# Performance work log

Hardware: AMD Instinct MI355X
Metric: run time of the kernel (lower is better)

The kernel has to match this reference:

```python
import jax, jax.numpy as jnp
import numpy as np

SOS_TOKEN = 1


def gru_cell(x, h, Wih, Whh, bih, bhh):
    # torch.nn.GRU gate math; x:[B,H], h:[B,H]; Wih/Whh:[3H,H]
    gi = x @ Wih.T + bih
    gh = h @ Whh.T + bhh
    ir, iz, inn = jnp.split(gi, 3, axis=-1)
    hr, hz, hn = jnp.split(gh, 3, axis=-1)
    r = jax.nn.sigmoid(ir + hr)
    z = jax.nn.sigmoid(iz + hz)
    n = jnp.tanh(inn + r * hn)
    return (1.0 - z) * n + z * h


def setup_inputs() -> dict:
    key = jax.random.key(0)
    ks = jax.random.split(key, 20)
    B, S, T, V, H = 32, 512, 128, 32000, 512
    sc = 0.08
    p = lambda i, shape: (jax.random.normal(ks[i], shape, jnp.float32) * sc)
    return {
        "input_seq": jax.random.randint(ks[0], (B, S), 0, V),
        "target_seq": jax.random.randint(ks[1], (B, T), 0, V),
        "emb": p(2, (V, H)),
        "ef_Wih": p(3, (3 * H, H)), "ef_Whh": p(4, (3 * H, H)),
        "ef_bih": p(5, (3 * H,)), "ef_bhh": p(6, (3 * H,)),
        "eb_Wih": p(7, (3 * H, H)), "eb_Whh": p(8, (3 * H, H)),
        "eb_bih": p(9, (3 * H,)), "eb_bhh": p(10, (3 * H,)),
        "d_Wih": p(11, (3 * H, H)), "d_Whh": p(12, (3 * H, H)),
        "d_bih": p(13, (3 * H,)), "d_bhh": p(14, (3 * H,)),
        "att_W": p(15, (H, 2 * H)), "att_b": p(16, (H,)),
        "out_W": p(17, (V, H)), "out_b": p(18, (V,)),
    }


def reference(input_seq, target_seq, emb,
              ef_Wih, ef_Whh, ef_bih, ef_bhh,
              eb_Wih, eb_Whh, eb_bih, eb_bhh,
              d_Wih, d_Whh, d_bih, d_bhh,
              att_W, att_b, out_W, out_b):
    B, S = input_seq.shape
    T = target_seq.shape[1]
    H = emb.shape[1]
    dtype = emb.dtype

    # ---- encoder: bidirectional GRU over source ----
    xs = jnp.swapaxes(emb[input_seq], 0, 1)  # [S,B,H]
    h0 = jnp.zeros((B, H), dtype)

    def make_step(Wih, Whh, bih, bhh):
        def f(h, xt):
            hn = gru_cell(xt, h, Wih, Whh, bih, bhh)
            return hn, hn
        return f

    hf_last, out_f = jax.lax.scan(make_step(ef_Wih, ef_Whh, ef_bih, ef_bhh), h0, xs)
    hb_last, out_bwd = jax.lax.scan(make_step(eb_Wih, eb_Whh, eb_bih, eb_bhh), h0, xs[::-1])
    out_bwd = out_bwd[::-1]
    # encoder_output[:, :H] + encoder_output[:, H:]  == sum of directions
    enc_out = jnp.swapaxes(out_f + out_bwd, 0, 1)  # [B,S,H]
    # decoder_hidden = encoder_hidden[-1,0] + encoder_hidden[-1,1]
    h_dec0 = hf_last + hb_last  # [B,H]

    # ---- greedy decode for T steps with argmax feedback ----
    tgt = target_seq.T  # [T,B]
    tok0 = jnp.full((B,), SOS_TOKEN, target_seq.dtype)
    batch_idx = jnp.arange(B)

    def dec_step(carry, tgt_t):
        h, tok, loss = carry
        xt = emb[tok]                                   # [B,H]
        hn = gru_cell(xt, h, d_Wih, d_Whh, d_bih, d_bhh)
        scores = jnp.einsum('bh,bsh->bs', hn, enc_out)  # dot attention
        w = jax.nn.softmax(scores, axis=-1)
        ctx = jnp.einsum('bs,bsh->bh', w, enc_out)
        att_out = jnp.tanh(jnp.concatenate([ctx, hn], axis=-1) @ att_W.T + att_b)
        logits = att_out @ out_W.T + out_b              # [B,V]
        logp = jax.nn.log_softmax(logits, axis=-1)
        loss = loss - logp[batch_idx, tgt_t]            # -log softmax(output)[target]
        nxt = jnp.argmax(logits, axis=-1).astype(tok.dtype)
        return (hn, nxt, loss), None

    init = (h_dec0, tok0, jnp.zeros((B,), dtype))
    (_, _, loss), _ = jax.lax.scan(dec_step, init, tgt)
    # mean over examples of (per-example loss / decoding_cnt)
    return jnp.mean(loss / T)
```

## Files before the change

kernel.cpp:

```cpp
#include <hip/hip_runtime.h>
#include <math.h>

#define B 32
#define S 512
#define T 128
#define V 32000
#define H 512
#define NB 256
#define NT 256
#define LCHUNK 250
#define LROWS 128
#define LDSPITCH 264

__device__ __forceinline__ float dot4(float acc, float4 a, float4 b){
    return fmaf(a.x,b.x, fmaf(a.y,b.y, fmaf(a.z,b.z, fmaf(a.w,b.w, acc))));
}
__device__ __forceinline__ float sigmoidf_(float x){ return 1.0f/(1.0f+expf(-x)); }

template<int GRPSZ>
__device__ __forceinline__ void gbar_arrive(unsigned* bb, unsigned grp, unsigned n){
    __syncthreads();
    if (threadIdx.x == 0){
        const unsigned r = __hip_atomic_fetch_add(bb + grp*32, 1u,
                              __ATOMIC_RELEASE, __HIP_MEMORY_SCOPE_AGENT);
        if (r == n*(unsigned)GRPSZ - 1u){
            const unsigned q = __hip_atomic_fetch_add(bb + 256, 1u,
                                  __ATOMIC_RELEASE, __HIP_MEMORY_SCOPE_AGENT);
            if (q == n*8u - 1u)
                __hip_atomic_store(bb + 288, n,
                                   __ATOMIC_RELEASE, __HIP_MEMORY_SCOPE_AGENT);
        }
    }
}
__device__ __forceinline__ void gbar_wait(unsigned* bb, unsigned n){
    if (threadIdx.x == 0){
        long guard = 0;
        while (__hip_atomic_load(bb + 288, __ATOMIC_RELAXED, __HIP_MEMORY_SCOPE_AGENT) < n){
            __builtin_amdgcn_s_sleep(2);
            if (++guard > 200000000L) break;
        }
        (void)__hip_atomic_load(bb + 288, __ATOMIC_ACQUIRE, __HIP_MEMORY_SCOPE_AGENT);
    }
    __syncthreads();
}

__global__ __launch_bounds__(NT, 1) void enc_persistent(
    const int* __restrict__ input_seq, const float* __restrict__ emb,
    const float* __restrict__ fWih, const float* __restrict__ fWhh,
    const float* __restrict__ fbih, const float* __restrict__ fbhh,
    const float* __restrict__ bWih, const float* __restrict__ bWhh,
    const float* __restrict__ bbih, const float* __restrict__ bbhh,
    float* enc_out, float* out_b, unsigned* bars)
{
    __shared__ float wlds[24*512];
    __shared__ float shp[128*6];
    const int bk = blockIdx.x, tid = threadIdx.x;
    const int dir = bk & 1, jg = bk >> 1;
    const int b = tid & 31, jj = (tid>>5)&3, kh = tid>>7;
    const int j = jg*4 + jj;
    const unsigned grp = ((unsigned)jg) & 7u;

    const float *Wih = dir? bWih : fWih;
    const float *Whh = dir? bWhh : fWhh;
    const float *bih = dir? bbih : fbih;
    const float *bhh = dir? bbhh : fbhh;
    float* outp = dir? out_b : enc_out;
    unsigned* bar = bars + dir*1024;

    for (int r=0;r<24;r++){
        const int jr = jg*4 + (r/6);
        const int g  = r % 6;
        const float* src = (g<3) ? (Wih + ((size_t)g*H + jr)*H)
                                 : (Whh + ((size_t)(g-3)*H + jr)*H);
        for (int k=tid;k<H;k+=NT) wlds[r*512+k] = src[k];
    }
    __syncthreads();

    const float4* wx0 = (const float4*)(wlds + (jj*6+0)*512 + kh*256);
    const float4* wx1 = (const float4*)(wlds + (jj*6+1)*512 + kh*256);
    const float4* wx2 = (const float4*)(wlds + (jj*6+2)*512 + kh*256);
    const float4* wh0 = (const float4*)(wlds + (jj*6+3)*512 + kh*256);
    const float4* wh1 = (const float4*)(wlds + (jj*6+4)*512 + kh*256);
    const float4* wh2 = (const float4*)(wlds + (jj*6+5)*512 + kh*256);
    const float bi_r = bih[j], bi_z = bih[H+j], bi_n = bih[2*H+j];
    const float bh_r = bhh[j], bh_z = bhh[H+j], bh_n = bhh[2*H+j];

    for (int t=0; t<S; t++){
        const int pos  = dir ? (S-1-t) : t;
        const int hpos = dir ? (S-t)   : (t-1);
        const int tokb = input_seq[b*S + pos];
        const float4* x4 = (const float4*)(emb + (size_t)tokb*H + kh*256);

        float ir=0.f, iz=0.f, in_=0.f;
        #pragma unroll 4
        for (int k=0;k<64;k++){
            const float4 xv = x4[k];
            ir  = dot4(ir , xv, wx0[k]);
            iz  = dot4(iz , xv, wx1[k]);
            in_ = dot4(in_, xv, wx2[k]);
        }

        if (t > 0) gbar_wait(bar, (unsigned)t);

        float hr=0.f, hz=0.f, hn=0.f;
        if (t > 0){
            const float4* h4 = (const float4*)(outp + ((size_t)b*S + hpos)*H + kh*256);
            #pragma unroll 4
            for (int k=0;k<64;k++){
                const float4 hv = h4[k];
                hr = dot4(hr, hv, wh0[k]);
                hz = dot4(hz, hv, wh1[k]);
                hn = dot4(hn, hv, wh2[k]);
            }
        }
        if (kh){
            float* p = shp + (jj*32 + b)*6;
            p[0]=ir; p[1]=iz; p[2]=in_; p[3]=hr; p[4]=hz; p[5]=hn;
        }
        __syncthreads();
        if (!kh){
            const float* p = shp + (jj*32 + b)*6;
            ir+=p[0]; iz+=p[1]; in_+=p[2]; hr+=p[3]; hz+=p[4]; hn+=p[5];
            float hprev = (t>0) ? outp[((size_t)b*S + hpos)*H + j] : 0.0f;
            const float r = sigmoidf_(ir + bi_r + hr + bh_r);
            const float z = sigmoidf_(iz + bi_z + hz + bh_z);
            const float n = tanhf(in_ + bi_n + r*(hn + bh_n));
            outp[((size_t)b*S + pos)*H + j] = (1.0f - z)*n + z*hprev;
        }
        gbar_arrive<16>(bar, grp, (unsigned)(t+1));
    }
}

__global__ __launch_bounds__(NT, 1) void dec_persistent(
    const int* __restrict__ target_seq, const float* __restrict__ emb,
    const float* __restrict__ dWih, const float* __restrict__ dWhh,
    const float* __restrict__ dbih, const float* __restrict__ dbhh,
    const float* __restrict__ attW, const float* __restrict__ attb,
    const float* __restrict__ outW, const float* __restrict__ outBias,
    float* enc_out, const float* out_b,
    float* hdec, float* scores, float* ctxb, float* att_out,
    float* pm, float* ps, int* pidx, float* lossb,
    float* out, unsigned* bar)
{
    __shared__ __align__(16) float smem[32*LDSPITCH];
    __shared__ float wg[12*512];
    __shared__ float wp[2*1024];
    __shared__ int sh_tok[B];
    const int bk = blockIdx.x, tid = threadIdx.x;
    const unsigned grp = (unsigned)bk & 7u;
    unsigned bn = 1;
#define GSYNC() do { gbar_arrive<32>(bar, grp, bn); gbar_wait(bar, bn); ++bn; } while(0)

    for (int r=0;r<12;r++){
        const int jr = bk*2 + (r/6);
        const int g  = r % 6;
        const float* src = (g<3) ? (dWih + ((size_t)g*H + jr)*H)
                                 : (dWhh + ((size_t)(g-3)*H + jr)*H);
        for (int k=tid;k<H;k+=NT) wg[r*512+k] = src[k];
    }
    for (int r=0;r<2;r++){
        const float* src = attW + (size_t)(bk*2+r)*(2*H);
        for (int k=tid;k<2*H;k+=NT) wp[r*1024+k] = src[k];
    }

    {
        const int gid = bk*NT + tid;
        if (gid < B*H){
            const int bb = gid >> 9, jq = gid & 511;
            hdec[gid] = enc_out[((size_t)bb*S + (S-1))*H + jq] + out_b[((size_t)bb*S)*H + jq];
        }
        if (bk==0 && tid<B) lossb[tid] = 0.0f;
    }
    GSYNC();

    {
        float4* e4 = (float4*)enc_out; const float4* o4 = (const float4*)out_b;
        for (size_t i = (size_t)bk*NT + tid; i < (size_t)B*S*H/4; i += (size_t)NB*NT){
            float4 x = e4[i]; const float4 y = o4[i];
            x.x+=y.x; x.y+=y.y; x.z+=y.z; x.w+=y.w; e4[i]=x;
        }
    }
    GSYNC();

    const int gb = tid & 31, gj = (tid>>5)&1, gkq = tid>>6;
    const int jrow = bk*2 + gj;
    const float4* gwir = (const float4*)(wg + (gj*6+0)*512 + gkq*128);
    const float4* gwiz = (const float4*)(wg + (gj*6+1)*512 + gkq*128);
    const float4* gwin = (const float4*)(wg + (gj*6+2)*512 + gkq*128);
    const float4* gwhr = (const float4*)(wg + (gj*6+3)*512 + gkq*128);
    const float4* gwhz = (const float4*)(wg + (gj*6+4)*512 + gkq*128);
    const float4* gwhn = (const float4*)(wg + (gj*6+5)*512 + gkq*128);
    const float gbi_r = dbih[jrow], gbi_z = dbih[H+jrow], gbi_n = dbih[2*H+jrow];
    const float gbh_r = dbhh[jrow], gbh_z = dbhh[H+jrow], gbh_n = dbhh[2*H+jrow];
    const float4* pw = (const float4*)(wp + gj*1024 + gkq*256);

    for (int t=0; t<T; t++){
        float* hin  = hdec + (size_t)(t&1)*B*H;
        float* hout = hdec + (size_t)((t+1)&1)*B*H;

        if (t == 0){
            if (tid < B) sh_tok[tid] = 1;
        } else {
            const int mb = tid>>3, p = tid&7;
            float bv = -INFINITY; int ai = 0x7FFFFFFF;
            for (int c=p; c<LCHUNK; c+=8){
                const float v = pm[mb*LCHUNK + c];
                if (v > bv){ bv = v; ai = pidx[mb*LCHUNK + c]; }
            }
            #pragma unroll
            for (int m=1; m<8; m<<=1){
                const float ov = __shfl_xor(bv, m); const int oi = __shfl_xor(ai, m);
                if (ov > bv || (ov == bv && oi < ai)){ bv = ov; ai = oi; }
            }
            if (p==0) sh_tok[mb] = ai;
            if (bk == 0){
                float mm = -INFINITY;
                for (int c=p; c<LCHUNK; c+=8) mm = fmaxf(mm, pm[mb*LCHUNK+c]);
                #pragma unroll
                for (int m=1;m<8;m<<=1) mm = fmaxf(mm, __shfl_xor(mm, m));
                float se = 0.0f;
                for (int c=p; c<LCHUNK; c+=8) se += ps[mb*LCHUNK+c]*expf(pm[mb*LCHUNK+c]-mm);
                #pragma unroll
                for (int m=1;m<8;m<<=1) se += __shfl_xor(se, m);
                const int tg = target_seq[mb*T + (t-1)];
                const float4* ar = (const float4*)(att_out + (size_t)mb*H) + p*16;
                const float4* wr = (const float4*)(outW + (size_t)tg*H) + p*16;
                float d = 0.0f;
                #pragma unroll
                for (int k=0;k<16;k++) d = dot4(d, ar[k], wr[k]);
                #pragma unroll
                for (int m=1;m<8;m<<=1) d += __shfl_xor(d, m);
                if (p==0) lossb[mb] += (mm + logf(se)) - (d + outBias[tg]);
            }
        }
        __syncthreads();
        {
            const int tokb = sh_tok[gb];
            const float4* x4 = (const float4*)(emb + (size_t)tokb*H + gkq*128);
            const float4* h4 = (const float4*)(hin + (size_t)gb*H + gkq*128);
            float ir=0.f, iz=0.f, in_=0.f, hr=0.f, hz=0.f, hn=0.f;
            #pragma unroll 4
            for (int k=0;k<32;k++){
                const float4 xv = x4[k], hv = h4[k];
                ir  = dot4(ir , xv, gwir[k]);
                iz  = dot4(iz , xv, gwiz[k]);
                in_ = dot4(in_, xv, gwin[k]);
                hr  = dot4(hr , hv, gwhr[k]);
                hz  = dot4(hz , hv, gwhz[k]);
                hn  = dot4(hn , hv, gwhn[k]);
            }
            if (gkq){
                float* pp = smem + ((gkq-1)*64 + gj*32 + gb)*6;
                pp[0]=ir; pp[1]=iz; pp[2]=in_; pp[3]=hr; pp[4]=hz; pp[5]=hn;
            }
            __syncthreads();
            if (!gkq){
                #pragma unroll
                for (int q=0;q<3;q++){
                    const float* pp = smem + (q*64 + gj*32 + gb)*6;
                    ir+=pp[0]; iz+=pp[1]; in_+=pp[2]; hr+=pp[3]; hz+=pp[4]; hn+=pp[5];
                }
                const float r = sigmoidf_(ir + gbi_r + hr + gbh_r);
                const float z = sigmoidf_(iz + gbi_z + hz + gbh_z);
                const float n = tanhf(in_ + gbi_n + r*(hn + gbh_n));
                const float hprev = hin[(size_t)gb*H + jrow];
                hout[(size_t)gb*H + jrow] = (1.0f - z)*n + z*hprev;
            }
        }
        GSYNC();

        {
            const int bS = bk & 31, sg = bk >> 5;
            const int sl = tid>>2, q = tid&3;
            const int s = sg*64 + sl;
            const float4* h4 = (const float4*)(hout + (size_t)bS*H + q*128);
            const float4* e4 = (const float4*)(enc_out + ((size_t)bS*S + s)*H + q*128);
            float a = 0.f;
            #pragma unroll 8
            for (int k=0;k<32;k++) a = dot4(a, h4[k], e4[k]);
            a += __shfl_xor(a, 1);
            a += __shfl_xor(a, 2);
            if (q == 0) scores[bS*S + s] = a;
        }
        GSYNC();

        {
            const int bC = bk & 31, cg = bk >> 5;
            float* sh_w = smem; float* red = smem + 512; float* part = smem + 768;
            const float s0 = scores[bC*S + tid], s1 = scores[bC*S + tid + 256];
            red[tid] = fmaxf(s0,s1); __syncthreads();
            for (int off=128; off>0; off>>=1){ if (tid<off) red[tid]=fmaxf(red[tid],red[tid+off]); __syncthreads(); }
            const float M = red[0]; __syncthreads();
            const float e0 = expf(s0-M), e1 = expf(s1-M);
            red[tid] = e0+e1; __syncthreads();
            for (int off=128; off>0; off>>=1){ if (tid<off) red[tid]+=red[tid+off]; __syncthreads(); }
            const float inv = 1.0f/red[0];
            __syncthreads();
            sh_w[tid] = e0*inv; sh_w[tid+256] = e1*inv;
            __syncthreads();
            const int col = cg*64 + (tid & 63);
            const int sg2 = tid >> 6;
            const float* Ec = enc_out + (size_t)bC*S*H + col;
            float acc = 0.f;
            #pragma unroll 8
            for (int s2=sg2; s2<S; s2+=4) acc = fmaf(sh_w[s2], Ec[(size_t)s2*H], acc);
            part[tid] = acc; __syncthreads();
            if (tid < 64) ctxb[bC*512 + col] = part[tid]+part[tid+64]+part[tid+128]+part[tid+192];
        }
        GSYNC();

        {
            const float* act = (gkq < 2) ? (ctxb + (size_t)gb*512 + gkq*256)
                                         : (hout + (size_t)gb*H + (gkq-2)*256);
            const float4* a4 = (const float4*)act;
            float acc = 0.f;
            #pragma unroll 8
            for (int k=0;k<64;k++) acc = dot4(acc, a4[k], pw[k]);
            if (gkq){
                smem[(gkq-1)*64 + gj*32 + gb] = acc;
            }
            __syncthreads();
            if (!gkq){
                acc += smem[0*64 + gj*32 + gb] + smem[1*64 + gj*32 + gb] + smem[2*64 + gj*32 + gb];
                att_out[(size_t)gb*H + jrow] = tanhf(acc + attb[jrow]);
            }
        }
        GSYNC();

        if (bk < LCHUNK){
            const int rg = tid & 31, bg = tid >> 5;
            const int r0 = bk*LROWS + rg;
            const float4* w0 = (const float4*)(outW + (size_t)(r0     )*H);
            const float4* w1 = (const float4*)(outW + (size_t)(r0 + 32)*H);
            const float4* w2 = (const float4*)(outW + (size_t)(r0 + 64)*H);
            const float4* w3 = (const float4*)(outW + (size_t)(r0 + 96)*H);
            float4* sh4 = (float4*)smem;
            float acc[4][4];
            #pragma unroll
            for (int i=0;i<4;i++){ acc[i][0]=0.f; acc[i][1]=0.f; acc[i][2]=0.f; acc[i][3]=0.f; }

            for (int ph=0; ph<2; ph++){
                #pragma unroll
                for (int ii=0; ii<8; ii++){
                    const int f4 = tid + 256*ii;
                    const int bb = f4 >> 6, k4 = f4 & 63;
                    sh4[bb*(LDSPITCH/4) + k4] = ((const float4*)att_out)[(size_t)bb*(H/4) + ph*64 + k4];
                }
                __syncthreads();
                #pragma unroll 4
                for (int k=0;k<64;k++){
                    const float4 a0 = sh4[(bg*4+0)*(LDSPITCH/4) + k];
                    const float4 a1 = sh4[(bg*4+1)*(LDSPITCH/4) + k];
                    const float4 a2 = sh4[(bg*4+2)*(LDSPITCH/4) + k];
                    const float4 a3 = sh4[(bg*4+3)*(LDSPITCH/4) + k];
                    const int kk = ph*64 + k;
                    {   const float4 wv = w0[kk];
                        acc[0][0]=dot4(acc[0][0],wv,a0); acc[0][1]=dot4(acc[0][1],wv,a1);
                        acc[0][2]=dot4(acc[0][2],wv,a2); acc[0][3]=dot4(acc[0][3],wv,a3); }
                    {   const float4 wv = w1[kk];
                        acc[1][0]=dot4(acc[1][0],wv,a0); acc[1][1]=dot4(acc[1][1],wv,a1);
                        acc[1][2]=dot4(acc[1][2],wv,a2); acc[1][3]=dot4(acc[1][3],wv,a3); }
                    {   const float4 wv = w2[kk];
                        acc[2][0]=dot4(acc[2][0],wv,a0); acc[2][1]=dot4(acc[2][1],wv,a1);
                        acc[2][2]=dot4(acc[2][2],wv,a2); acc[2][3]=dot4(acc[2][3],wv,a3); }
                    {   const float4 wv = w3[kk];
                        acc[3][0]=dot4(acc[3][0],wv,a0); acc[3][1]=dot4(acc[3][1],wv,a1);
                        acc[3][2]=dot4(acc[3][2],wv,a2); acc[3][3]=dot4(acc[3][3],wv,a3); }
                }
                __syncthreads();
            }

            const float bias0 = outBias[r0], bias1 = outBias[r0+32], bias2 = outBias[r0+64], bias3 = outBias[r0+96];
            #pragma unroll
            for (int jb=0;jb<4;jb++){
                float l0 = acc[0][jb]+bias0, l1 = acc[1][jb]+bias1, l2 = acc[2][jb]+bias2, l3 = acc[3][jb]+bias3;
                float M = fmaxf(fmaxf(l0,l1), fmaxf(l2,l3));
                #pragma unroll
                for (int m=1;m<32;m<<=1) M = fmaxf(M, __shfl_xor(M, m));
                float sum = expf(l0-M)+expf(l1-M)+expf(l2-M)+expf(l3-M);
                #pragma unroll
                for (int m=1;m<32;m<<=1) sum += __shfl_xor(sum, m);
                float bv = l0; int bi = r0;
                if (l1 > bv){ bv=l1; bi=r0+32; }
                if (l2 > bv){ bv=l2; bi=r0+64; }
                if (l3 > bv){ bv=l3; bi=r0+96; }
                #pragma unroll
                for (int m=1;m<32;m<<=1){
                    const float ov = __shfl_xor(bv, m); const int oi = __shfl_xor(bi, m);
                    if (ov > bv || (ov == bv && oi < bi)){ bv=ov; bi=oi; }
                }
                if (rg == 0){
                    const int bb = bg*4 + jb;
                    pm[bb*LCHUNK + bk] = M;
                    ps[bb*LCHUNK + bk] = sum;
                    pidx[bb*LCHUNK + bk] = bi;
                }
            }
        }
        GSYNC();
    }

    if (bk == 0){
        const int mb = tid>>3, p = tid&7;
        float mm = -INFINITY;
        for (int c=p; c<LCHUNK; c+=8) mm = fmaxf(mm, pm[mb*LCHUNK+c]);
        #pragma unroll
        for (int m=1;m<8;m<<=1) mm = fmaxf(mm, __shfl_xor(mm, m));
        float se = 0.0f;
        for (int c=p; c<LCHUNK; c+=8) se += ps[mb*LCHUNK+c]*expf(pm[mb*LCHUNK+c]-mm);
        #pragma unroll
        for (int m=1;m<8;m<<=1) se += __shfl_xor(se, m);
        const int tg = target_seq[mb*T + (T-1)];
        const float4* ar = (const float4*)(att_out + (size_t)mb*H) + p*16;
        const float4* wr = (const float4*)(outW + (size_t)tg*H) + p*16;
        float d = 0.0f;
        #pragma unroll
        for (int k=0;k<16;k++) d = dot4(d, ar[k], wr[k]);
        #pragma unroll
        for (int m=1;m<8;m<<=1) d += __shfl_xor(d, m);
        if (p==0) lossb[mb] += (mm + logf(se)) - (d + outBias[tg]);
        __syncthreads();
        if (tid < B){
            float v = lossb[tid];
            for (int off=16; off>0; off>>=1) v += __shfl_down(v, off);
            if (tid == 0) out[0] = v / (float)(B*T);
        }
    }
#undef GSYNC
}

extern "C" void kernel_launch(void* const* d_in, const int* in_sizes, int n_in,
                              void* d_out, int out_size, void* d_ws, size_t ws_size,
                              hipStream_t stream)
{
    const int*   input_seq  = (const int*)  d_in[0];
    const int*   target_seq = (const int*)  d_in[1];
    const float* emb    = (const float*)d_in[2];
    const float* efWih  = (const float*)d_in[3];
    const float* efWhh  = (const float*)d_in[4];
    const float* efbih  = (const float*)d_in[5];
    const float* efbhh  = (const float*)d_in[6];
    const float* ebWih  = (const float*)d_in[7];
    const float* ebWhh  = (const float*)d_in[8];
    const float* ebbih  = (const float*)d_in[9];
    const float* ebbhh  = (const float*)d_in[10];
    const float* dWih   = (const float*)d_in[11];
    const float* dWhh   = (const float*)d_in[12];
    const float* dbih   = (const float*)d_in[13];
    const float* dbhh   = (const float*)d_in[14];
    const float* attW   = (const float*)d_in[15];
    const float* attb   = (const float*)d_in[16];
    const float* outW   = (const float*)d_in[17];
    const float* outBias= (const float*)d_in[18];

    float* ws      = (float*)d_ws;
    unsigned* bars = (unsigned*)ws;
    float* enc_out = ws + 4096;
    float* outb    = enc_out + (size_t)B*S*H;
    float* scores  = outb    + (size_t)B*S*H;
    float* ctxb    = scores  + (size_t)B*S;
    float* attout  = ctxb    + (size_t)B*512;
    float* pm      = attout  + (size_t)B*H;
    float* ps      = pm      + (size_t)B*LCHUNK;
    int*   pidx    = (int*)(ps + (size_t)B*LCHUNK);
    float* hdec    = (float*)(pidx + (size_t)B*LCHUNK);
    float* lossb   = hdec    + (size_t)2*B*H;

    hipMemsetAsync(bars, 0, 16384, stream);

    enc_persistent<<<NB, NT, 0, stream>>>(input_seq, emb,
        efWih, efWhh, efbih, efbhh, ebWih, ebWhh, ebbih, ebbhh,
        enc_out, outb, bars);

    dec_persistent<<<NB, NT, 0, stream>>>(target_seq, emb,
        dWih, dWhh, dbih, dbhh, attW, attb, outW, outBias,
        enc_out, outb, hdec, scores, ctxb, attout,
        pm, ps, pidx, lossb, (float*)d_out, bars + 2048);
}
```

Measured before the change: 32.41 ms.

## Double threads per block and split reduction dimensions across more threads

Raises the block size of the persistent encoder and decoder kernels from 256 to 512 threads. Each phase (GRU gate dot products, attention scores, softmax/context, attention projection, vocab logits) is re-partitioned so each thread covers half as much of the K or S dimension, with larger shared-memory partial reductions. The aim is to shorten the per-step critical path of these latency-bound recurrent loops by adding intra-block parallelism. The cost is more shared-memory reduction work and possible register or occupancy pressure, and some sections must now guard threads 256 and above.

```diff
diff --git a/kernel.cpp b/kernel.cpp
--- a/kernel.cpp
+++ b/kernel.cpp
@@ -7,7 +7,7 @@
 #define V 32000
 #define H 512
 #define NB 256
-#define NT 256
+#define NT 512
 #define LCHUNK 250
 #define LROWS 128
 #define LDSPITCH 264
@@ -53,7 +53,7 @@
     float* enc_out, float* out_b, unsigned* bars)
 {
     __shared__ float wlds[24*512];
-    __shared__ float shp[128*6];
+    __shared__ float shp[3*128*6];
     const int bk = blockIdx.x, tid = threadIdx.x;
     const int dir = bk & 1, jg = bk >> 1;
     const int b = tid & 31, jj = (tid>>5)&3, kh = tid>>7;
@@ -76,12 +76,12 @@
     }
     __syncthreads();
 
-    const float4* wx0 = (const float4*)(wlds + (jj*6+0)*512 + kh*256);
-    const float4* wx1 = (const float4*)(wlds + (jj*6+1)*512 + kh*256);
-    const float4* wx2 = (const float4*)(wlds + (jj*6+2)*512 + kh*256);
-    const float4* wh0 = (const float4*)(wlds + (jj*6+3)*512 + kh*256);
-    const float4* wh1 = (const float4*)(wlds + (jj*6+4)*512 + kh*256);
-    const float4* wh2 = (const float4*)(wlds + (jj*6+5)*512 + kh*256);
+    const float4* wx0 = (const float4*)(wlds + (jj*6+0)*512 + kh*128);
+    const float4* wx1 = (const float4*)(wlds + (jj*6+1)*512 + kh*128);
+    const float4* wx2 = (const float4*)(wlds + (jj*6+2)*512 + kh*128);
+    const float4* wh0 = (const float4*)(wlds + (jj*6+3)*512 + kh*128);
+    const float4* wh1 = (const float4*)(wlds + (jj*6+4)*512 + kh*128);
+    const float4* wh2 = (const float4*)(wlds + (jj*6+5)*512 + kh*128);
     const float bi_r = bih[j], bi_z = bih[H+j], bi_n = bih[2*H+j];
     const float bh_r = bhh[j], bh_z = bhh[H+j], bh_n = bhh[2*H+j];
 
@@ -89,11 +89,11 @@
         const int pos  = dir ? (S-1-t) : t;
         const int hpos = dir ? (S-t)   : (t-1);
         const int tokb = input_seq[b*S + pos];
-        const float4* x4 = (const float4*)(emb + (size_t)tokb*H + kh*256);
+        const float4* x4 = (const float4*)(emb + (size_t)tokb*H + kh*128);
 
         float ir=0.f, iz=0.f, in_=0.f;
-        #pragma unroll 4
-        for (int k=0;k<64;k++){
+        #pragma unroll 8
+        for (int k=0;k<32;k++){
             const float4 xv = x4[k];
             ir  = dot4(ir , xv, wx0[k]);
             iz  = dot4(iz , xv, wx1[k]);
@@ -104,9 +104,9 @@
 
         float hr=0.f, hz=0.f, hn=0.f;
         if (t > 0){
-            const float4* h4 = (const float4*)(outp + ((size_t)b*S + hpos)*H + kh*256);
-            #pragma unroll 4
-            for (int k=0;k<64;k++){
+            const float4* h4 = (const float4*)(outp + ((size_t)b*S + hpos)*H + kh*128);
+            #pragma unroll 8
+            for (int k=0;k<32;k++){
                 const float4 hv = h4[k];
                 hr = dot4(hr, hv, wh0[k]);
                 hz = dot4(hz, hv, wh1[k]);
@@ -114,13 +114,16 @@
             }
         }
         if (kh){
-            float* p = shp + (jj*32 + b)*6;
+            float* p = shp + ((kh-1)*128 + jj*32 + b)*6;
             p[0]=ir; p[1]=iz; p[2]=in_; p[3]=hr; p[4]=hz; p[5]=hn;
         }
         __syncthreads();
         if (!kh){
-            const float* p = shp + (jj*32 + b)*6;
-            ir+=p[0]; iz+=p[1]; in_+=p[2]; hr+=p[3]; hz+=p[4]; hn+=p[5];
+            #pragma unroll
+            for (int q=0;q<3;q++){
+                const float* p = shp + (q*128 + jj*32 + b)*6;
+                ir+=p[0]; iz+=p[1]; in_+=p[2]; hr+=p[3]; hz+=p[4]; hn+=p[5];
+            }
             float hprev = (t>0) ? outp[((size_t)b*S + hpos)*H + j] : 0.0f;
             const float r = sigmoidf_(ir + bi_r + hr + bh_r);
             const float z = sigmoidf_(iz + bi_z + hz + bh_z);
@@ -184,15 +187,15 @@
 
     const int gb = tid & 31, gj = (tid>>5)&1, gkq = tid>>6;
     const int jrow = bk*2 + gj;
-    const float4* gwir = (const float4*)(wg + (gj*6+0)*512 + gkq*128);
-    const float4* gwiz = (const float4*)(wg + (gj*6+1)*512 + gkq*128);
-    const float4* gwin = (const float4*)(wg + (gj*6+2)*512 + gkq*128);
-    const float4* gwhr = (const float4*)(wg + (gj*6+3)*512 + gkq*128);
-    const float4* gwhz = (const float4*)(wg + (gj*6+4)*512 + gkq*128);
-    const float4* gwhn = (const float4*)(wg + (gj*6+5)*512 + gkq*128);
+    const float4* gwir = (const float4*)(wg + (gj*6+0)*512 + gkq*64);
+    const float4* gwiz = (const float4*)(wg + (gj*6+1)*512 + gkq*64);
+    const float4* gwin = (const float4*)(wg + (gj*6+2)*512 + gkq*64);
+    const float4* gwhr = (const float4*)(wg + (gj*6+3)*512 + gkq*64);
+    const float4* gwhz = (const float4*)(wg + (gj*6+4)*512 + gkq*64);
+    const float4* gwhn = (const float4*)(wg + (gj*6+5)*512 + gkq*64);
     const float gbi_r = dbih[jrow], gbi_z = dbih[H+jrow], gbi_n = dbih[2*H+jrow];
     const float gbh_r = dbhh[jrow], gbh_z = dbhh[H+jrow], gbh_n = dbhh[2*H+jrow];
-    const float4* pw = (const float4*)(wp + gj*1024 + gkq*256);
+    const float4* pw = (const float4*)(wp + gj*1024 + gkq*128);
 
     for (int t=0; t<T; t++){
         float* hin  = hdec + (size_t)(t&1)*B*H;
@@ -200,7 +203,7 @@
 
         if (t == 0){
             if (tid < B) sh_tok[tid] = 1;
-        } else {
+        } else if (tid < 256) {
             const int mb = tid>>3, p = tid&7;
             float bv = -INFINITY; int ai = 0x7FFFFFFF;
             for (int c=p; c<LCHUNK; c+=8){
@@ -236,11 +239,11 @@
         __syncthreads();
         {
             const int tokb = sh_tok[gb];
-            const float4* x4 = (const float4*)(emb + (size_t)tokb*H + gkq*128);
-            const float4* h4 = (const float4*)(hin + (size_t)gb*H + gkq*128);
+            const float4* x4 = (const float4*)(emb + (size_t)tokb*H + gkq*64);
+            const float4* h4 = (const float4*)(hin + (size_t)gb*H + gkq*64);
             float ir=0.f, iz=0.f, in_=0.f, hr=0.f, hz=0.f, hn=0.f;
-            #pragma unroll 4
-            for (int k=0;k<32;k++){
+            #pragma unroll
+            for (int k=0;k<16;k++){
                 const float4 xv = x4[k], hv = h4[k];
                 ir  = dot4(ir , xv, gwir[k]);
                 iz  = dot4(iz , xv, gwiz[k]);
@@ -256,7 +259,7 @@
             __syncthreads();
             if (!gkq){
                 #pragma unroll
-                for (int q=0;q<3;q++){
+                for (int q=0;q<7;q++){
                     const float* pp = smem + (q*64 + gj*32 + gb)*6;
                     ir+=pp[0]; iz+=pp[1]; in_+=pp[2]; hr+=pp[3]; hz+=pp[4]; hn+=pp[5];
                 }
@@ -271,57 +274,64 @@
 
         {
             const int bS = bk & 31, sg = bk >> 5;
-            const int sl = tid>>2, q = tid&3;
+            const int sl = tid>>3, q = tid&7;
             const int s = sg*64 + sl;
-            const float4* h4 = (const float4*)(hout + (size_t)bS*H + q*128);
-            const float4* e4 = (const float4*)(enc_out + ((size_t)bS*S + s)*H + q*128);
+            const float4* h4 = (const float4*)(hout + (size_t)bS*H + q*64);
+            const float4* e4 = (const float4*)(enc_out + ((size_t)bS*S + s)*H + q*64);
             float a = 0.f;
-            #pragma unroll 8
-            for (int k=0;k<32;k++) a = dot4(a, h4[k], e4[k]);
+            #pragma unroll
+            for (int k=0;k<16;k++) a = dot4(a, h4[k], e4[k]);
             a += __shfl_xor(a, 1);
             a += __shfl_xor(a, 2);
+            a += __shfl_xor(a, 4);
             if (q == 0) scores[bS*S + s] = a;
         }
         GSYNC();
 
         {
             const int bC = bk & 31, cg = bk >> 5;
-            float* sh_w = smem; float* red = smem + 512; float* part = smem + 768;
-            const float s0 = scores[bC*S + tid], s1 = scores[bC*S + tid + 256];
-            red[tid] = fmaxf(s0,s1); __syncthreads();
-            for (int off=128; off>0; off>>=1){ if (tid<off) red[tid]=fmaxf(red[tid],red[tid+off]); __syncthreads(); }
+            float* sh_w = smem; float* red = smem + 512; float* part = smem + 1024;
+            const float s0 = scores[bC*S + tid];
+            red[tid] = s0; __syncthreads();
+            for (int off=256; off>0; off>>=1){ if (tid<off) red[tid]=fmaxf(red[tid],red[tid+off]); __syncthreads(); }
             const float M = red[0]; __syncthreads();
-            const float e0 = expf(s0-M), e1 = expf(s1-M);
-            red[tid] = e0+e1; __syncthreads();
-            for (int off=128; off>0; off>>=1){ if (tid<off) red[tid]+=red[tid+off]; __syncthreads(); }
+            const float e0 = expf(s0-M);
+            red[tid] = e0; __syncthreads();
+            for (int off=256; off>0; off>>=1){ if (tid<off) red[tid]+=red[tid+off]; __syncthreads(); }
             const float inv = 1.0f/red[0];
             __syncthreads();
-            sh_w[tid] = e0*inv; sh_w[tid+256] = e1*inv;
+            sh_w[tid] = e0*inv;
             __syncthreads();
             const int col = cg*64 + (tid & 63);
             const int sg2 = tid >> 6;
             const float* Ec = enc_out + (size_t)bC*S*H + col;
             float acc = 0.f;
             #pragma unroll 8
-            for (int s2=sg2; s2<S; s2+=4) acc = fmaf(sh_w[s2], Ec[(size_t)s2*H], acc);
+            for (int s2=sg2; s2<S; s2+=8) acc = fmaf(sh_w[s2], Ec[(size_t)s2*H], acc);
             part[tid] = acc; __syncthreads();
-            if (tid < 64) ctxb[bC*512 + col] = part[tid]+part[tid+64]+part[tid+128]+part[tid+192];
+            if (tid < 64){
+                float v = 0.f;
+                #pragma unroll
+                for (int i=0;i<8;i++) v += part[tid + 64*i];
+                ctxb[bC*512 + cg*64 + tid] = v;
+            }
         }
         GSYNC();
 
         {
-            const float* act = (gkq < 2) ? (ctxb + (size_t)gb*512 + gkq*256)
-                                         : (hout + (size_t)gb*H + (gkq-2)*256);
+            const float* act = (gkq < 4) ? (ctxb + (size_t)gb*512 + gkq*128)
+                                         : (hout + (size_t)gb*H + (gkq-4)*128);
             const float4* a4 = (const float4*)act;
             float acc = 0.f;
-            #pragma unroll 8
-            for (int k=0;k<64;k++) acc = dot4(acc, a4[k], pw[k]);
+            #pragma unroll
+            for (int k=0;k<32;k++) acc = dot4(acc, a4[k], pw[k]);
             if (gkq){
                 smem[(gkq-1)*64 + gj*32 + gb] = acc;
             }
             __syncthreads();
             if (!gkq){
-                acc += smem[0*64 + gj*32 + gb] + smem[1*64 + gj*32 + gb] + smem[2*64 + gj*32 + gb];
+                #pragma unroll
+                for (int q=0;q<7;q++) acc += smem[q*64 + gj*32 + gb];
                 att_out[(size_t)gb*H + jrow] = tanhf(acc + attb[jrow]);
             }
         }
@@ -335,44 +345,38 @@
             const float4* w2 = (const float4*)(outW + (size_t)(r0 + 64)*H);
             const float4* w3 = (const float4*)(outW + (size_t)(r0 + 96)*H);
             float4* sh4 = (float4*)smem;
-            float acc[4][4];
-            #pragma unroll
-            for (int i=0;i<4;i++){ acc[i][0]=0.f; acc[i][1]=0.f; acc[i][2]=0.f; acc[i][3]=0.f; }
+            float acc[4][2];
+            #pragma unroll
+            for (int i=0;i<4;i++){ acc[i][0]=0.f; acc[i][1]=0.f; }
 
             for (int ph=0; ph<2; ph++){
                 #pragma unroll
-                for (int ii=0; ii<8; ii++){
-                    const int f4 = tid + 256*ii;
+                for (int ii=0; ii<4; ii++){
+                    const int f4 = tid + 512*ii;
                     const int bb = f4 >> 6, k4 = f4 & 63;
                     sh4[bb*(LDSPITCH/4) + k4] = ((const float4*)att_out)[(size_t)bb*(H/4) + ph*64 + k4];
                 }
                 __syncthreads();
                 #pragma unroll 4
                 for (int k=0;k<64;k++){
-                    const float4 a0 = sh4[(bg*4+0)*(LDSPITCH/4) + k];
-                    const float4 a1 = sh4[(bg*4+1)*(LDSPITCH/4) + k];
-                    const float4 a2 = sh4[(bg*4+2)*(LDSPITCH/4) + k];
-                    const float4 a3 = sh4[(bg*4+3)*(LDSPITCH/4) + k];
+                    const float4 a0 = sh4[(bg*2+0)*(LDSPITCH/4) + k];
+                    const float4 a1 = sh4[(bg*2+1)*(LDSPITCH/4) + k];
                     const int kk = ph*64 + k;
                     {   const float4 wv = w0[kk];
-                        acc[0][0]=dot4(acc[0][0],wv,a0); acc[0][1]=dot4(acc[0][1],wv,a1);
-                        acc[0][2]=dot4(acc[0][2],wv,a2); acc[0][3]=dot4(acc[0][3],wv,a3); }
+                        acc[0][0]=dot4(acc[0][0],wv,a0); acc[0][1]=dot4(acc[0][1],wv,a1); }
                     {   const float4 wv = w1[kk];
-                        acc[1][0]=dot4(acc[1][0],wv,a0); acc[1][1]=dot4(acc[1][1],wv,a1);
-                        acc[1][2]=dot4(acc[1][2],wv,a2); acc[1][3]=dot4(acc[1][3],wv,a3); }
+                        acc[1][0]=dot4(acc[1][0],wv,a0); acc[1][1]=dot4(acc[1][1],wv,a1); }
                     {   const float4 wv = w2[kk];
-                        acc[2][0]=dot4(acc[2][0],wv,a0); acc[2][1]=dot4(acc[2][1],wv,a1);
-                        acc[2][2]=dot4(acc[2][2],wv,a2); acc[2][3]=dot4(acc[2][3],wv,a3); }
+                        acc[2][0]=dot4(acc[2][0],wv,a0); acc[2][1]=dot4(acc[2][1],wv,a1); }
                     {   const float4 wv = w3[kk];
-                        acc[3][0]=dot4(acc[3][0],wv,a0); acc[3][1]=dot4(acc[3][1],wv,a1);
-                        acc[3][2]=dot4(acc[3][2],wv,a2); acc[3][3]=dot4(acc[3][3],wv,a3); }
+                        acc[3][0]=dot4(acc[3][0],wv,a0); acc[3][1]=dot4(acc[3][1],wv,a1); }
                 }
                 __syncthreads();
             }
 
             const float bias0 = outBias[r0], bias1 = outBias[r0+32], bias2 = outBias[r0+64], bias3 = outBias[r0+96];
             #pragma unroll
-            for (int jb=0;jb<4;jb++){
+            for (int jb=0;jb<2;jb++){
                 float l0 = acc[0][jb]+bias0, l1 = acc[1][jb]+bias1, l2 = acc[2][jb]+bias2, l3 = acc[3][jb]+bias3;
                 float M = fmaxf(fmaxf(l0,l1), fmaxf(l2,l3));
                 #pragma unroll
@@ -390,7 +394,7 @@
                     if (ov > bv || (ov == bv && oi < bi)){ bv=ov; bi=oi; }
                 }
                 if (rg == 0){
-                    const int bb = bg*4 + jb;
+                    const int bb = bg*2 + jb;
                     pm[bb*LCHUNK + bk] = M;
                     ps[bb*LCHUNK + bk] = sum;
                     pidx[bb*LCHUNK + bk] = bi;
@@ -401,24 +405,26 @@
     }
 
     if (bk == 0){
-        const int mb = tid>>3, p = tid&7;
-        float mm = -INFINITY;
-        for (int c=p; c<LCHUNK; c+=8) mm = fmaxf(mm, pm[mb*LCHUNK+c]);
-        #pragma unroll
-        for (int m=1;m<8;m<<=1) mm = fmaxf(mm, __shfl_xor(mm, m));
-        float se = 0.0f;
-        for (int c=p; c<LCHUNK; c+=8) se += ps[mb*LCHUNK+c]*expf(pm[mb*LCHUNK+c]-mm);
-        #pragma unroll
-        for (int m=1;m<8;m<<=1) se += __shfl_xor(se, m);
-        const int tg = target_seq[mb*T + (T-1)];
-        const float4* ar = (const float4*)(att_out + (size_t)mb*H) + p*16;
-        const float4* wr = (const float4*)(outW + (size_t)tg*H) + p*16;
-        float d = 0.0f;
-        #pragma unroll
-        for (int k=0;k<16;k++) d = dot4(d, ar[k], wr[k]);
-        #pragma unroll
-        for (int m=1;m<8;m<<=1) d += __shfl_xor(d, m);
-        if (p==0) lossb[mb] += (mm + logf(se)) - (d + outBias[tg]);
+        if (tid < 256){
+            const int mb = tid>>3, p = tid&7;
+            float mm = -INFINITY;
+            for (int c=p; c<LCHUNK; c+=8) mm = fmaxf(mm, pm[mb*LCHUNK+c]);
+            #pragma unroll
+            for (int m=1;m<8;m<<=1) mm = fmaxf(mm, __shfl_xor(mm, m));
+            float se = 0.0f;
+            for (int c=p; c<LCHUNK; c+=8) se += ps[mb*LCHUNK+c]*expf(pm[mb*LCHUNK+c]-mm);
+            #pragma unroll
+            for (int m=1;m<8;m<<=1) se += __shfl_xor(se, m);
+            const int tg = target_seq[mb*T + (T-1)];
+            const float4* ar = (const float4*)(att_out + (size_t)mb*H) + p*16;
+            const float4* wr = (const float4*)(outW + (size_t)tg*H) + p*16;
+            float d = 0.0f;
+            #pragma unroll
+            for (int k=0;k<16;k++) d = dot4(d, ar[k], wr[k]);
+            #pragma unroll
+            for (int m=1;m<8;m<<=1) d += __shfl_xor(d, m);
+            if (p==0) lossb[mb] += (mm + logf(se)) - (d + outBias[tg]);
+        }
         __syncthreads();
         if (tid < B){
             float v = lossb[tid];
```

Measured after the change: 37.35 ms. +15.3%, slower.

## Widen encoder K-split to four ways and restructure vocab projection tiling

Applied to the files above, without the earlier changes.

The encoder now uses 512 threads per block, splitting each GRU dot product into four K-quarters instead of two, which shortens the serial per-step latency of the recurrence. The output-vocab projection loads the whole att_out into LDS once in k-major layout, with no two-phase staging. Each thread now covers four consecutive vocab rows for four batches. The softmax/argmax reduction becomes an online max-sum merge across 8-lane shuffles plus a cross-wave LDS reduction. The risks are more LDS use, bank conflicts from the new layouts, and extra reduction steps in exchange for fewer barriers and better coalescing of outW rows.

```diff
diff --git a/kernel.cpp b/kernel.cpp
--- a/kernel.cpp
+++ b/kernel.cpp
@@ -7,10 +7,10 @@
 #define V 32000
 #define H 512
 #define NB 256
-#define NT 256
+#define NTE 512
+#define NTD 256
 #define LCHUNK 250
 #define LROWS 128
-#define LDSPITCH 264
 
 __device__ __forceinline__ float dot4(float acc, float4 a, float4 b){
     return fmaf(a.x,b.x, fmaf(a.y,b.y, fmaf(a.z,b.z, fmaf(a.w,b.w, acc))));
@@ -44,7 +44,7 @@
     __syncthreads();
 }
 
-__global__ __launch_bounds__(NT, 1) void enc_persistent(
+__global__ __launch_bounds__(NTE, 1) void enc_persistent(
     const int* __restrict__ input_seq, const float* __restrict__ emb,
     const float* __restrict__ fWih, const float* __restrict__ fWhh,
     const float* __restrict__ fbih, const float* __restrict__ fbhh,
@@ -53,7 +53,7 @@
     float* enc_out, float* out_b, unsigned* bars)
 {
     __shared__ float wlds[24*512];
-    __shared__ float shp[128*6];
+    __shared__ float shp[3*128*6];
     const int bk = blockIdx.x, tid = threadIdx.x;
     const int dir = bk & 1, jg = bk >> 1;
     const int b = tid & 31, jj = (tid>>5)&3, kh = tid>>7;
@@ -72,16 +72,16 @@
         const int g  = r % 6;
         const float* src = (g<3) ? (Wih + ((size_t)g*H + jr)*H)
                                  : (Whh + ((size_t)(g-3)*H + jr)*H);
-        for (int k=tid;k<H;k+=NT) wlds[r*512+k] = src[k];
+        for (int k=tid;k<H;k+=NTE) wlds[r*512+k] = src[k];
     }
     __syncthreads();
 
-    const float4* wx0 = (const float4*)(wlds + (jj*6+0)*512 + kh*256);
-    const float4* wx1 = (const float4*)(wlds + (jj*6+1)*512 + kh*256);
-    const float4* wx2 = (const float4*)(wlds + (jj*6+2)*512 + kh*256);
-    const float4* wh0 = (const float4*)(wlds + (jj*6+3)*512 + kh*256);
-    const float4* wh1 = (const float4*)(wlds + (jj*6+4)*512 + kh*256);
-    const float4* wh2 = (const float4*)(wlds + (jj*6+5)*512 + kh*256);
+    const float4* wx0 = (const float4*)(wlds + (jj*6+0)*512 + kh*128);
+    const float4* wx1 = (const float4*)(wlds + (jj*6+1)*512 + kh*128);
+    const float4* wx2 = (const float4*)(wlds + (jj*6+2)*512 + kh*128);
+    const float4* wh0 = (const float4*)(wlds + (jj*6+3)*512 + kh*128);
+    const float4* wh1 = (const float4*)(wlds + (jj*6+4)*512 + kh*128);
+    const float4* wh2 = (const float4*)(wlds + (jj*6+5)*512 + kh*128);
     const float bi_r = bih[j], bi_z = bih[H+j], bi_n = bih[2*H+j];
     const float bh_r = bhh[j], bh_z = bhh[H+j], bh_n = bhh[2*H+j];
 
@@ -89,11 +89,11 @@
         const int pos  = dir ? (S-1-t) : t;
         const int hpos = dir ? (S-t)   : (t-1);
         const int tokb = input_seq[b*S + pos];
-        const float4* x4 = (const float4*)(emb + (size_t)tokb*H + kh*256);
+        const float4* x4 = (const float4*)(emb + (size_t)tokb*H + kh*128);
 
         float ir=0.f, iz=0.f, in_=0.f;
-        #pragma unroll 4
-        for (int k=0;k<64;k++){
+        #pragma unroll 8
+        for (int k=0;k<32;k++){
             const float4 xv = x4[k];
             ir  = dot4(ir , xv, wx0[k]);
             iz  = dot4(iz , xv, wx1[k]);
@@ -104,9 +104,9 @@
 
         float hr=0.f, hz=0.f, hn=0.f;
         if (t > 0){
-            const float4* h4 = (const float4*)(outp + ((size_t)b*S + hpos)*H + kh*256);
-            #pragma unroll 4
-            for (int k=0;k<64;k++){
+            const float4* h4 = (const float4*)(outp + ((size_t)b*S + hpos)*H + kh*128);
+            #pragma unroll 8
+            for (int k=0;k<32;k++){
                 const float4 hv = h4[k];
                 hr = dot4(hr, hv, wh0[k]);
                 hz = dot4(hz, hv, wh1[k]);
@@ -114,13 +114,16 @@
             }
         }
         if (kh){
-            float* p = shp + (jj*32 + b)*6;
+            float* p = shp + ((kh-1)*128 + jj*32 + b)*6;
             p[0]=ir; p[1]=iz; p[2]=in_; p[3]=hr; p[4]=hz; p[5]=hn;
         }
         __syncthreads();
         if (!kh){
-            const float* p = shp + (jj*32 + b)*6;
-            ir+=p[0]; iz+=p[1]; in_+=p[2]; hr+=p[3]; hz+=p[4]; hn+=p[5];
+            #pragma unroll
+            for (int q=0;q<3;q++){
+                const float* p = shp + (q*128 + jj*32 + b)*6;
+                ir+=p[0]; iz+=p[1]; in_+=p[2]; hr+=p[3]; hz+=p[4]; hn+=p[5];
+            }
             float hprev = (t>0) ? outp[((size_t)b*S + hpos)*H + j] : 0.0f;
             const float r = sigmoidf_(ir + bi_r + hr + bh_r);
             const float z = sigmoidf_(iz + bi_z + hz + bh_z);
@@ -131,7 +134,7 @@
     }
 }
 
-__global__ __launch_bounds__(NT, 1) void dec_persistent(
+__global__ __launch_bounds__(NTD, 1) void dec_persistent(
     const int* __restrict__ target_seq, const float* __restrict__ emb,
     const float* __restrict__ dWih, const float* __restrict__ dWhh,
     const float* __restrict__ dbih, const float* __restrict__ dbhh,
@@ -142,9 +145,11 @@
     float* pm, float* ps, int* pidx, float* lossb,
     float* out, unsigned* bar)
 {
-    __shared__ __align__(16) float smem[32*LDSPITCH];
+    __shared__ __align__(16) float smem[128*32*4];
     __shared__ float wg[12*512];
     __shared__ float wp[2*1024];
+    __shared__ float red_m[4][32], red_s[4][32];
+    __shared__ int   red_i[4][32];
     __shared__ int sh_tok[B];
     const int bk = blockIdx.x, tid = threadIdx.x;
     const unsigned grp = (unsigned)bk & 7u;
@@ -156,15 +161,15 @@
         const int g  = r % 6;
         const float* src = (g<3) ? (dWih + ((size_t)g*H + jr)*H)
                                  : (dWhh + ((size_t)(g-3)*H + jr)*H);
-        for (int k=tid;k<H;k+=NT) wg[r*512+k] = src[k];
+        for (int k=tid;k<H;k+=NTD) wg[r*512+k] = src[k];
     }
     for (int r=0;r<2;r++){
         const float* src = attW + (size_t)(bk*2+r)*(2*H);
-        for (int k=tid;k<2*H;k+=NT) wp[r*1024+k] = src[k];
+        for (int k=tid;k<2*H;k+=NTD) wp[r*1024+k] = src[k];
     }
 
     {
-        const int gid = bk*NT + tid;
+        const int gid = bk*NTD + tid;
         if (gid < B*H){
             const int bb = gid >> 9, jq = gid & 511;
             hdec[gid] = enc_out[((size_t)bb*S + (S-1))*H + jq] + out_b[((size_t)bb*S)*H + jq];
@@ -175,7 +180,7 @@
 
     {
         float4* e4 = (float4*)enc_out; const float4* o4 = (const float4*)out_b;
-        for (size_t i = (size_t)bk*NT + tid; i < (size_t)B*S*H/4; i += (size_t)NB*NT){
+        for (size_t i = (size_t)bk*NTD + tid; i < (size_t)B*S*H/4; i += (size_t)NB*NTD){
             float4 x = e4[i]; const float4 y = o4[i];
             x.x+=y.x; x.y+=y.y; x.z+=y.z; x.w+=y.w; e4[i]=x;
         }
@@ -328,73 +333,80 @@
         GSYNC();
 
         if (bk < LCHUNK){
-            const int rg = tid & 31, bg = tid >> 5;
-            const int r0 = bk*LROWS + rg;
-            const float4* w0 = (const float4*)(outW + (size_t)(r0     )*H);
-            const float4* w1 = (const float4*)(outW + (size_t)(r0 + 32)*H);
-            const float4* w2 = (const float4*)(outW + (size_t)(r0 + 64)*H);
-            const float4* w3 = (const float4*)(outW + (size_t)(r0 + 96)*H);
             float4* sh4 = (float4*)smem;
+            for (int idx = tid; idx < 32*128; idx += NTD){
+                const int k4 = idx & 127, bb = idx >> 7;
+                sh4[k4*32 + bb] = ((const float4*)att_out)[(size_t)bb*128 + k4];
+            }
+            __syncthreads();
+            const int wid = tid >> 6, lane = tid & 63;
+            const int rl = lane & 7, bl = lane >> 3;
+            const int r0 = bk*LROWS + wid*32 + rl*4;
+            const float4* w0 = (const float4*)(outW + (size_t)(r0+0)*H);
+            const float4* w1 = (const float4*)(outW + (size_t)(r0+1)*H);
+            const float4* w2 = (const float4*)(outW + (size_t)(r0+2)*H);
+            const float4* w3 = (const float4*)(outW + (size_t)(r0+3)*H);
             float acc[4][4];
             #pragma unroll
             for (int i=0;i<4;i++){ acc[i][0]=0.f; acc[i][1]=0.f; acc[i][2]=0.f; acc[i][3]=0.f; }
-
-            for (int ph=0; ph<2; ph++){
-                #pragma unroll
-                for (int ii=0; ii<8; ii++){
-                    const int f4 = tid + 256*ii;
-                    const int bb = f4 >> 6, k4 = f4 & 63;
-                    sh4[bb*(LDSPITCH/4) + k4] = ((const float4*)att_out)[(size_t)bb*(H/4) + ph*64 + k4];
+            #pragma unroll 4
+            for (int k=0;k<128;k++){
+                const float4 a0 = sh4[k*32 + bl*4 + 0];
+                const float4 a1 = sh4[k*32 + bl*4 + 1];
+                const float4 a2 = sh4[k*32 + bl*4 + 2];
+                const float4 a3 = sh4[k*32 + bl*4 + 3];
+                {   const float4 wv = w0[k];
+                    acc[0][0]=dot4(acc[0][0],wv,a0); acc[0][1]=dot4(acc[0][1],wv,a1);
+                    acc[0][2]=dot4(acc[0][2],wv,a2); acc[0][3]=dot4(acc[0][3],wv,a3); }
+                {   const float4 wv = w1[k];
+                    acc[1][0]=dot4(acc[1][0],wv,a0); acc[1][1]=dot4(acc[1][1],wv,a1);
+                    acc[1][2]=dot4(acc[1][2],wv,a2); acc[1][3]=dot4(acc[1][3],wv,a3); }
+                {   const float4 wv = w2[k];
+                    acc[2][0]=dot4(acc[2][0],wv,a0); acc[2][1]=dot4(acc[2][1],wv,a1);
+                    acc[2][2]=dot4(acc[2][2],wv,a2); acc[2][3]=dot4(acc[2][3],wv,a3); }
+                {   const float4 wv = w3[k];
+                    acc[3][0]=dot4(acc[3][0],wv,a0); acc[3][1]=dot4(acc[3][1],wv,a1);
+                    acc[3][2]=dot4(acc[3][2],wv,a2); acc[3][3]=dot4(acc[3][3],wv,a3); }
+            }
+            const float bs0 = outBias[r0], bs1 = outBias[r0+1], bs2 = outBias[r0+2], bs3 = outBias[r0+3];
+            #pragma unroll
+            for (int j=0;j<4;j++){
+                const float l0 = acc[0][j]+bs0, l1 = acc[1][j]+bs1, l2 = acc[2][j]+bs2, l3 = acc[3][j]+bs3;
+                float M = l0; int bi = r0;
+                if (l1 > M){ M=l1; bi=r0+1; }
+                if (l2 > M){ M=l2; bi=r0+2; }
+                if (l3 > M){ M=l3; bi=r0+3; }
+                float Ssum = expf(l0-M)+expf(l1-M)+expf(l2-M)+expf(l3-M);
+                #pragma unroll
+                for (int m=1;m<8;m<<=1){
+                    const float oM = __shfl_xor(M, m);
+                    const float oS = __shfl_xor(Ssum, m);
+                    const int   oI = __shfl_xor(bi, m);
+                    const float nM = fmaxf(M, oM);
+                    const float nS = Ssum*expf(M-nM) + oS*expf(oM-nM);
+                    if (oM > M || (oM == M && oI < bi)) bi = oI;
+                    M = nM; Ssum = nS;
                 }
-                __syncthreads();
-                #pragma unroll 4
-                for (int k=0;k<64;k++){
-                    const float4 a0 = sh4[(bg*4+0)*(LDSPITCH/4) + k];
-                    const float4 a1 = sh4[(bg*4+1)*(LDSPITCH/4) + k];
-                    const float4 a2 = sh4[(bg*4+2)*(LDSPITCH/4) + k];
-                    const float4 a3 = sh4[(bg*4+3)*(LDSPITCH/4) + k];
-                    const int kk = ph*64 + k;
-                    {   const float4 wv = w0[kk];
-                        acc[0][0]=dot4(acc[0][0],wv,a0); acc[0][1]=dot4(acc[0][1],wv,a1);
-                        acc[0][2]=dot4(acc[0][2],wv,a2); acc[0][3]=dot4(acc[0][3],wv,a3); }
-                    {   const float4 wv = w1[kk];
-                        acc[1][0]=dot4(acc[1][0],wv,a0); acc[1][1]=dot4(acc[1][1],wv,a1);
-                        acc[1][2]=dot4(acc[1][2],wv,a2); acc[1][3]=dot4(acc[1][3],wv,a3); }
-                    {   const float4 wv = w2[kk];
-                        acc[2][0]=dot4(acc[2][0],wv,a0); acc[2][1]=dot4(acc[2][1],wv,a1);
-                        acc[2][2]=dot4(acc[2][2],wv,a2); acc[2][3]=dot4(acc[2][3],wv,a3); }
-                    {   const float4 wv = w3[kk];
-                        acc[3][0]=dot4(acc[3][0],wv,a0); acc[3][1]=dot4(acc[3][1],wv,a1);
-                        acc[3][2]=dot4(acc[3][2],wv,a2); acc[3][3]=dot4(acc[3][3],wv,a3); }
+                if (rl == 0){
+                    red_m[wid][bl*4+j] = M;
+                    red_s[wid][bl*4+j] = Ssum;
+                    red_i[wid][bl*4+j] = bi;
                 }
-                __syncthreads();
-            }
-
-            const float bias0 = outBias[r0], bias1 = outBias[r0+32], bias2 = outBias[r0+64], bias3 = outBias[r0+96];
-            #pragma unroll
-            for (int jb=0;jb<4;jb++){
-                float l0 = acc[0][jb]+bias0, l1 = acc[1][jb]+bias1, l2 = acc[2][jb]+bias2, l3 = acc[3][jb]+bias3;
-                float M = fmaxf(fmaxf(l0,l1), fmaxf(l2,l3));
-                #pragma unroll
-                for (int m=1;m<32;m<<=1) M = fmaxf(M, __shfl_xor(M, m));
-                float sum = expf(l0-M)+expf(l1-M)+expf(l2-M)+expf(l3-M);
-                #pragma unroll
-                for (int m=1;m<32;m<<=1) sum += __shfl_xor(sum, m);
-                float bv = l0; int bi = r0;
-                if (l1 > bv){ bv=l1; bi=r0+32; }
-                if (l2 > bv){ bv=l2; bi=r0+64; }
-                if (l3 > bv){ bv=l3; bi=r0+96; }
-                #pragma unroll
-                for (int m=1;m<32;m<<=1){
-                    const float ov = __shfl_xor(bv, m); const int oi = __shfl_xor(bi, m);
-                    if (ov > bv || (ov == bv && oi < bi)){ bv=ov; bi=oi; }
+            }
+            __syncthreads();
+            if (tid < 32){
+                float M = red_m[0][tid], Ssum = red_s[0][tid]; int bi = red_i[0][tid];
+                #pragma unroll
+                for (int w=1; w<4; w++){
+                    const float oM = red_m[w][tid], oS = red_s[w][tid]; const int oI = red_i[w][tid];
+                    const float nM = fmaxf(M, oM);
+                    const float nS = Ssum*expf(M-nM) + oS*expf(oM-nM);
+                    if (oM > M || (oM == M && oI < bi)) bi = oI;
+                    M = nM; Ssum = nS;
                 }
-                if (rg == 0){
-                    const int bb = bg*4 + jb;
-                    pm[bb*LCHUNK + bk] = M;
-                    ps[bb*LCHUNK + bk] = sum;
-                    pidx[bb*LCHUNK + bk] = bi;
-                }
+                pm[tid*LCHUNK + bk] = M;
+                ps[tid*LCHUNK + bk] = Ssum;
+                pidx[tid*LCHUNK + bk] = bi;
             }
         }
         GSYNC();
@@ -468,11 +480,11 @@
 
     hipMemsetAsync(bars, 0, 16384, stream);
 
-    enc_persistent<<<NB, NT, 0, stream>>>(input_seq, emb,
+    enc_persistent<<<NB, NTE, 0, stream>>>(input_seq, emb,
         efWih, efWhh, efbih, efbhh, ebWih, ebWhh, ebbih, ebbhh,
         enc_out, outb, bars);
 
-    dec_persistent<<<NB, NT, 0, stream>>>(target_seq, emb,
+    dec_persistent<<<NB, NTD, 0, stream>>>(target_seq, emb,
         dWih, dWhh, dbih, dbhh, attW, attb, outW, outBias,
         enc_out, outb, hdec, scores, ctxb, attout,
         pm, ps, pidx, lossb, (float*)d_out, bars + 2048);
```

Result: no change. 31.84 ms (-1.7%).
